# Kernel tuning notes

Measured on AMD Instinct MI355X. Metric: run time of the kernel, lower is better.

Reference implementation:

```python
import jax, jax.numpy as jnp
import numpy as np

N = 100000
E = 3200000
H = 128
C = 40


def setup_inputs() -> dict:
    key = jax.random.key(0)
    ks = jax.random.split(key, 7)
    x = jax.random.normal(ks[0], (N, H), dtype=jnp.float32)
    edge_src = jax.random.randint(ks[1], (E,), 0, N, dtype=jnp.int32)
    edge_dst = jnp.sort(jax.random.randint(ks[2], (E,), 0, N, dtype=jnp.int32))
    edge_w = jax.random.uniform(ks[3], (E,), dtype=jnp.float32)
    s = 1.0 / np.sqrt(H)
    W0 = jax.random.normal(ks[4], (H, H), dtype=jnp.float32) * s
    W1 = jax.random.normal(ks[5], (H, H), dtype=jnp.float32) * s
    W2 = jax.random.normal(ks[6], (H, C), dtype=jnp.float32) * s
    return {"x": x, "edge_src": edge_src, "edge_dst": edge_dst,
            "edge_w": edge_w, "W0": W0, "W1": W1, "W2": W2}


def _spmm(h, edge_src, edge_dst, edge_w):
    # out[i] = sum_{e: dst_e == i} w_e * h[src_e]   (sparse adj @ h)
    msgs = h[edge_src] * edge_w[:, None]          # [E, d]
    return jax.ops.segment_sum(msgs, edge_dst, num_segments=N)


def reference(x, edge_src, edge_dst, edge_w, W0, W1, W2):
    # layer 1: tanh(Linear(spmm(adj, x)))  (dropout is identity in eval mode)
    h = jnp.tanh(_spmm(x, edge_src, edge_dst, edge_w) @ W0)
    # layer 2
    h = jnp.tanh(_spmm(h, edge_src, edge_dst, edge_w) @ W1)
    # output layer (GraphConvSparse default activation is tanh here too)
    out = jnp.tanh(_spmm(h, edge_src, edge_dst, edge_w) @ W2)
    return out
```

## Files before the change

### kernel.cpp

```cpp
#include <hip/hip_runtime.h>
#include <hip/hip_fp16.h>

#define NN 100000
#define NPAD 100096
#define EE 3200000
#define HH 128
#define CC 40
#define NT 16

typedef _Float16 f16x8 __attribute__((ext_vector_type(8)));
typedef float f32x4 __attribute__((ext_vector_type(4)));

#define EDEC_W(v) ((float)((v) >> 17) * (1.f / 32767.f))
#define EDEC_S(v) ((v) & 131071u)

__device__ __forceinline__ float fast_tanh(float x) {
    float t = __expf(2.f * fminf(x, 15.f));
    return (t - 1.f) * __builtin_amdgcn_rcpf(t + 1.f);
}

__global__ void build_rp(const int* __restrict__ dst, int* __restrict__ rp) {
    int i = blockIdx.x * blockDim.x + threadIdx.x;
    if (i > NN) return;
    int lo = 0, hi = EE;
    while (lo < hi) {
        int mid = (lo + hi) >> 1;
        if (dst[mid] < i) lo = mid + 1; else hi = mid;
    }
    rp[i] = lo;
}

__global__ __launch_bounds__(256) void prep_all(const float* __restrict__ x,
                                                const int* __restrict__ src,
                                                const float* __restrict__ w,
                                                const float* __restrict__ W0,
                                                const float* __restrict__ W1,
                                                const float* __restrict__ W2,
                                                __half* __restrict__ xh,
                                                unsigned* __restrict__ ewp,
                                                __half* __restrict__ W0t,
                                                __half* __restrict__ W1t,
                                                __half* __restrict__ W2t) {
    int b = blockIdx.x, tid = threadIdx.x;
    if (b < 6250) {
        int base = (b * 256 + tid) * 8;
        float4 a = *(const float4*)(x + base);
        float4 c = *(const float4*)(x + base + 4);
        __half2 h[4];
        h[0] = __floats2half2_rn(a.x, a.y);
        h[1] = __floats2half2_rn(a.z, a.w);
        h[2] = __floats2half2_rn(c.x, c.y);
        h[3] = __floats2half2_rn(c.z, c.w);
        *(float4*)(xh + base) = *(float4*)h;
    } else if (b < 9375) {
        int i = (b - 6250) * 256 + tid;
        int4 s = ((const int4*)src)[i];
        float4 f = ((const float4*)w)[i];
        uint4 p;
        p.x = (unsigned)s.x | ((unsigned)(f.x * 32767.f + 0.5f) << 17);
        p.y = (unsigned)s.y | ((unsigned)(f.y * 32767.f + 0.5f) << 17);
        p.z = (unsigned)s.z | ((unsigned)(f.z * 32767.f + 0.5f) << 17);
        p.w = (unsigned)s.w | ((unsigned)(f.w * 32767.f + 0.5f) << 17);
        ((uint4*)ewp)[i] = p;
    } else {
        int i = (b - 9375) * 256 + tid;
        if (i < HH * HH) {
            int c = i >> 7, k = i & 127;
            W0t[i] = __float2half_rn(W0[k * HH + c]);
            W1t[i] = __float2half_rn(W1[k * HH + c]);
        }
        if (i < 64 * HH) {
            int c = i >> 7, k = i & 127;
            W2t[i] = __float2half_rn(c < CC ? W2[k * CC + c] : 0.f);
        }
    }
}

__global__ __launch_bounds__(256) void sort_edges(const unsigned* __restrict__ in,
                                                  const int* __restrict__ rp,
                                                  unsigned* __restrict__ outp) {
    int node = blockIdx.x * 4 + (threadIdx.x >> 6);
    int l = threadIdx.x & 63;
    if (node >= NN) return;
    int e0 = __builtin_amdgcn_readfirstlane(rp[node]);
    int e1 = __builtin_amdgcn_readfirstlane(rp[node + 1]);
    int count[NT];
#pragma unroll
    for (int t = 0; t < NT; ++t) count[t] = 0;
    for (int e = e0; e < e1; e += 64) {
        int idx = e + l;
        bool val = idx < e1;
        unsigned v = val ? in[idx] : 0u;
        int t = val ? (int)(EDEC_S(v) >> 13) : -1;
#pragma unroll
        for (int tt = 0; tt < NT; ++tt)
            count[tt] += __popcll(__ballot(t == tt));
    }
    int base[NT];
    int run = e0;
#pragma unroll
    for (int tt = 0; tt < NT; ++tt) { base[tt] = run; run += count[tt]; }
    unsigned long long lmask = (1ull << l) - 1ull;
    for (int e = e0; e < e1; e += 64) {
        int idx = e + l;
        bool val = idx < e1;
        unsigned v = val ? in[idx] : 0u;
        int t = val ? (int)(EDEC_S(v) >> 13) : -1;
#pragma unroll
        for (int tt = 0; tt < NT; ++tt) {
            unsigned long long b = __ballot(t == tt);
            if (t == tt) outp[base[tt] + __popcll(b & lmask)] = v;
            base[tt] += __popcll(b);
        }
    }
}

__global__ __launch_bounds__(256) void spmm_h16(const __half* __restrict__ h,
                                                const unsigned* __restrict__ ewp,
                                                const int* __restrict__ rp,
                                                __half* __restrict__ out) {
    int node = blockIdx.x * 4 + (threadIdx.x >> 6);
    int l = threadIdx.x & 63;
    if (node >= NN) return;
    int e0 = __builtin_amdgcn_readfirstlane(rp[node]);
    int e1 = __builtin_amdgcn_readfirstlane(rp[node + 1]);
    int g = l >> 4, r = l & 15;
    const f16x8* __restrict__ hrow = (const f16x8*)h;
    float acc[8] = {};
    int e = e0;
    while ((e & 3) && e < e1) {
        unsigned v = ewp[e];
        float wk = (g == 0) ? EDEC_W(v) : 0.f;
        f16x8 vv = hrow[(size_t)EDEC_S(v) * 16 + r];
#pragma unroll
        for (int j = 0; j < 8; ++j) acc[j] = fmaf(wk, (float)vv[j], acc[j]);
        ++e;
    }
    int e16 = e + ((e1 - e) & ~15);
    for (; e < e16; e += 16) {
        uint4 p = *(const uint4*)(ewp + e + 4 * g);
        f16x8 v0 = hrow[(size_t)EDEC_S(p.x) * 16 + r];
        f16x8 v1 = hrow[(size_t)EDEC_S(p.y) * 16 + r];
        f16x8 v2 = hrow[(size_t)EDEC_S(p.z) * 16 + r];
        f16x8 v3 = hrow[(size_t)EDEC_S(p.w) * 16 + r];
        float w0 = EDEC_W(p.x), w1 = EDEC_W(p.y), w2 = EDEC_W(p.z), w3 = EDEC_W(p.w);
#pragma unroll
        for (int j = 0; j < 8; ++j) acc[j] = fmaf(w0, (float)v0[j], acc[j]);
#pragma unroll
        for (int j = 0; j < 8; ++j) acc[j] = fmaf(w1, (float)v1[j], acc[j]);
#pragma unroll
        for (int j = 0; j < 8; ++j) acc[j] = fmaf(w2, (float)v2[j], acc[j]);
#pragma unroll
        for (int j = 0; j < 8; ++j) acc[j] = fmaf(w3, (float)v3[j], acc[j]);
    }
    if (e < e1) {
#pragma unroll
        for (int k = 0; k < 4; ++k) {
            int idx = e + 4 * g + k;
            bool val = idx < e1;
            unsigned v = ewp[val ? idx : e0];
            float wk = val ? EDEC_W(v) : 0.f;
            f16x8 vv = hrow[(size_t)EDEC_S(v) * 16 + r];
#pragma unroll
            for (int j = 0; j < 8; ++j) acc[j] = fmaf(wk, (float)vv[j], acc[j]);
        }
    }
#pragma unroll
    for (int j = 0; j < 8; ++j) {
        acc[j] += __shfl_xor(acc[j], 16);
        acc[j] += __shfl_xor(acc[j], 32);
    }
    if (l < 16) {
        __half2 hv[4];
#pragma unroll
        for (int j = 0; j < 4; ++j) hv[j] = __floats2half2_rn(acc[2 * j], acc[2 * j + 1]);
        *(float4*)(out + (size_t)node * HH + r * 8) = *(float4*)hv;
    }
}

__global__ __launch_bounds__(256) void spmm40_tanh(const __half* __restrict__ gpad,
                                                   const unsigned* __restrict__ ewp,
                                                   const int* __restrict__ rp,
                                                   float* __restrict__ out) {
    int node = blockIdx.x * 4 + (threadIdx.x >> 6);
    int l = threadIdx.x & 63;
    if (node >= NN) return;
    int e0 = __builtin_amdgcn_readfirstlane(rp[node]);
    int e1 = __builtin_amdgcn_readfirstlane(rp[node + 1]);
    int g = l >> 3, r = l & 7;
    const f16x8* __restrict__ grw = (const f16x8*)gpad;
    float acc[8] = {};
    int e = e0;
    while ((e & 1) && e < e1) {
        unsigned v = ewp[e];
        float wk = (g == 0) ? EDEC_W(v) : 0.f;
        f16x8 vv = grw[(size_t)EDEC_S(v) * 8 + r];
#pragma unroll
        for (int j = 0; j < 8; ++j) acc[j] = fmaf(wk, (float)vv[j], acc[j]);
        ++e;
    }
    int e16 = e + ((e1 - e) & ~15);
    for (; e < e16; e += 16) {
        uint2 pa = *(const uint2*)(ewp + e + 2 * g);
        f16x8 v0 = grw[(size_t)EDEC_S(pa.x) * 8 + r];
        f16x8 v1 = grw[(size_t)EDEC_S(pa.y) * 8 + r];
        float w0 = EDEC_W(pa.x), w1 = EDEC_W(pa.y);
#pragma unroll
        for (int j = 0; j < 8; ++j) acc[j] = fmaf(w0, (float)v0[j], acc[j]);
#pragma unroll
        for (int j = 0; j < 8; ++j) acc[j] = fmaf(w1, (float)v1[j], acc[j]);
    }
    if (e < e1) {
#pragma unroll
        for (int k = 0; k < 2; ++k) {
            int idx = e + 2 * g + k;
            bool val = idx < e1;
            unsigned v = ewp[val ? idx : e0];
            float wk = val ? EDEC_W(v) : 0.f;
            f16x8 vv = grw[(size_t)EDEC_S(v) * 8 + r];
#pragma unroll
            for (int j = 0; j < 8; ++j) acc[j] = fmaf(wk, (float)vv[j], acc[j]);
        }
    }
#pragma unroll
    for (int j = 0; j < 8; ++j) {
        acc[j] += __shfl_xor(acc[j], 8);
        acc[j] += __shfl_xor(acc[j], 16);
        acc[j] += __shfl_xor(acc[j], 32);
    }
    if (l < 5) {
        float o[8];
#pragma unroll
        for (int j = 0; j < 8; ++j) o[j] = fast_tanh(acc[j]);
        *(float4*)(out + (size_t)node * CC + r * 8) = *(float4*)&o[0];
        *(float4*)(out + (size_t)node * CC + r * 8 + 4) = *(float4*)&o[4];
    }
}

__global__ __launch_bounds__(256) void gemm_tanh_mfma(const __half* __restrict__ A,
                                                      const __half* __restrict__ Wt,
                                                      __half* __restrict__ out) {
    __shared__ _Float16 st[4][16][136];
    int wave = threadIdx.x >> 6, l = threadIdx.x & 63;
    int r0 = blockIdx.x * 64 + wave * 16;
    int lr = l & 15, lg = l >> 4;
    const _Float16* Af = (const _Float16*)A;
    const _Float16* Wf = (const _Float16*)Wt;
    f16x8 a[4];
#pragma unroll
    for (int kb = 0; kb < 4; ++kb)
        a[kb] = *(const f16x8*)(Af + (size_t)(r0 + lr) * HH + kb * 32 + lg * 8);
#pragma unroll
    for (int ct = 0; ct < 8; ++ct) {
        f32x4 acc = {0.f, 0.f, 0.f, 0.f};
#pragma unroll
        for (int kb = 0; kb < 4; ++kb) {
            f16x8 b = *(const f16x8*)(Wf + (size_t)(ct * 16 + lr) * HH + kb * 32 + lg * 8);
            acc = __builtin_amdgcn_mfma_f32_16x16x32_f16(a[kb], b, acc, 0, 0, 0);
        }
#pragma unroll
        for (int r = 0; r < 4; ++r)
            st[wave][lg * 4 + r][ct * 16 + lr] = (_Float16)fast_tanh(acc[r]);
    }
#pragma unroll
    for (int i = 0; i < 4; ++i) {
        int row = lg + 4 * i;
        int grow = r0 + row;
        f16x8 v = *(const f16x8*)&st[wave][row][lr * 8];
        if (grow < NN)
            *(f16x8*)((_Float16*)out + (size_t)grow * HH + lr * 8) = v;
    }
}

__global__ __launch_bounds__(256) void gemm2_fused(const __half* __restrict__ A,
                                                   const __half* __restrict__ W1t,
                                                   const __half* __restrict__ W2t,
                                                   __half* __restrict__ gout) {
    __shared__ _Float16 st[4][16][136];
    int wave = threadIdx.x >> 6, l = threadIdx.x & 63;
    int r0 = blockIdx.x * 64 + wave * 16;
    int lr = l & 15, lg = l >> 4;
    const _Float16* Af = (const _Float16*)A;
    const _Float16* W1f = (const _Float16*)W1t;
    const _Float16* W2f = (const _Float16*)W2t;
    f16x8 a[4];
#pragma unroll
    for (int kb = 0; kb < 4; ++kb)
        a[kb] = *(const f16x8*)(Af + (size_t)(r0 + lr) * HH + kb * 32 + lg * 8);
#pragma unroll
    for (int ct = 0; ct < 8; ++ct) {
        f32x4 acc = {0.f, 0.f, 0.f, 0.f};
#pragma unroll
        for (int kb = 0; kb < 4; ++kb) {
            f16x8 b = *(const f16x8*)(W1f + (size_t)(ct * 16 + lr) * HH + kb * 32 + lg * 8);
            acc = __builtin_amdgcn_mfma_f32_16x16x32_f16(a[kb], b, acc, 0, 0, 0);
        }
#pragma unroll
        for (int r = 0; r < 4; ++r)
            st[wave][lg * 4 + r][ct * 16 + lr] = (_Float16)fast_tanh(acc[r]);
    }
    f16x8 a2[4];
#pragma unroll
    for (int kb = 0; kb < 4; ++kb)
        a2[kb] = *(const f16x8*)&st[wave][lr][kb * 32 + lg * 8];
#pragma unroll
    for (int ct = 0; ct < 4; ++ct) {
        f32x4 acc = {0.f, 0.f, 0.f, 0.f};
#pragma unroll
        for (int kb = 0; kb < 4; ++kb) {
            f16x8 b = *(const f16x8*)(W2f + (size_t)(ct * 16 + lr) * HH + kb * 32 + lg * 8);
            acc = __builtin_amdgcn_mfma_f32_16x16x32_f16(a2[kb], b, acc, 0, 0, 0);
        }
#pragma unroll
        for (int r = 0; r < 4; ++r)
            st[wave][lg * 4 + r][ct * 16 + lr] = (_Float16)acc[r];
    }
#pragma unroll
    for (int i = 0; i < 2; ++i) {
        int row = (l >> 3) + 8 * i;
        int grow = r0 + row;
        f16x8 v = *(const f16x8*)&st[wave][row][(l & 7) * 8];
        if (grow < NN)
            *(f16x8*)((_Float16*)gout + (size_t)grow * 64 + (l & 7) * 8) = v;
    }
}

extern "C" void kernel_launch(void* const* d_in, const int* in_sizes, int n_in,
                              void* d_out, int out_size, void* d_ws, size_t ws_size,
                              hipStream_t stream) {
    const float* x    = (const float*)d_in[0];
    const int*   esrc = (const int*)d_in[1];
    const int*   edst = (const int*)d_in[2];
    const float* ew_f = (const float*)d_in[3];
    const float* W0   = (const float*)d_in[4];
    const float* W1   = (const float*)d_in[5];
    const float* W2   = (const float*)d_in[6];
    float* out = (float*)d_out;

    char* ws = (char*)d_ws;
    size_t off = 0;
    int* rp = (int*)(ws + off);            off += (((size_t)(NN + 1) * 4) + 511) & ~(size_t)511;
    __half* buf0 = (__half*)(ws + off);    off += (size_t)NPAD * HH * sizeof(__half);
    __half* sA = (__half*)(ws + off);      off += (size_t)NPAD * HH * sizeof(__half);
    __half* hb = (__half*)(ws + off);      off += (size_t)NPAD * HH * sizeof(__half);
    unsigned* ewp = (unsigned*)(ws + off); off += (size_t)EE * sizeof(unsigned);
    unsigned* ews = (unsigned*)(ws + off); off += (size_t)EE * sizeof(unsigned);
    __half* W0t = (__half*)(ws + off);     off += (size_t)HH * HH * sizeof(__half);
    __half* W1t = (__half*)(ws + off);     off += (size_t)HH * HH * sizeof(__half);
    __half* W2t = (__half*)(ws + off);     off += (size_t)64 * HH * sizeof(__half);
    __half* xh = buf0;
    __half* gb = buf0;

    build_rp<<<(NN + 256) / 256, 256, 0, stream>>>(edst, rp);
    prep_all<<<9440, 256, 0, stream>>>(x, esrc, ew_f, W0, W1, W2,
                                       xh, ewp, W0t, W1t, W2t);
    sort_edges<<<NN / 4, 256, 0, stream>>>(ewp, rp, ews);

    int gemm_grid = NPAD / 64;
    spmm_h16<<<NN / 4, 256, 0, stream>>>(xh, ews, rp, sA);
    gemm_tanh_mfma<<<gemm_grid, 256, 0, stream>>>(sA, W0t, hb);
    spmm_h16<<<NN / 4, 256, 0, stream>>>(hb, ews, rp, sA);
    gemm2_fused<<<gemm_grid, 256, 0, stream>>>(sA, W1t, W2t, gb);
    spmm40_tanh<<<NN / 4, 256, 0, stream>>>(gb, ews, rp, out);
}
```

Before: 504.7 us.

## Fuse SpMM with dense GEMM per layer and drop the edge-sorting pass

Each of the first two layers now runs as one kernel: each 512-thread block aggregates 16 node rows into LDS, then applies the MFMA GEMM and tanh directly from LDS. This removes the intermediate sA buffer round-trips through global memory and two kernel launches. The row-pointer binary search moves into the prep kernel, and the per-node sort of edges by source tile is removed, which saves a full pass over the edge list. The cost is that gathers now follow the original edge order, so cache locality on the source-row reads may be worse.

```diff
diff --git a/kernel.cpp b/kernel.cpp
--- a/kernel.cpp
+++ b/kernel.cpp
@@ -2,13 +2,12 @@
 #include <hip/hip_fp16.h>
 
 #define NN 100000
-#define NPAD 100096
 #define EE 3200000
 #define HH 128
 #define CC 40
-#define NT 16
 
 typedef _Float16 f16x8 __attribute__((ext_vector_type(8)));
+typedef _Float16 f16x4 __attribute__((ext_vector_type(4)));
 typedef float f32x4 __attribute__((ext_vector_type(4)));
 
 #define EDEC_W(v) ((float)((v) >> 17) * (1.f / 32767.f))
@@ -19,19 +18,9 @@
     return (t - 1.f) * __builtin_amdgcn_rcpf(t + 1.f);
 }
 
-__global__ void build_rp(const int* __restrict__ dst, int* __restrict__ rp) {
-    int i = blockIdx.x * blockDim.x + threadIdx.x;
-    if (i > NN) return;
-    int lo = 0, hi = EE;
-    while (lo < hi) {
-        int mid = (lo + hi) >> 1;
-        if (dst[mid] < i) lo = mid + 1; else hi = mid;
-    }
-    rp[i] = lo;
-}
-
 __global__ __launch_bounds__(256) void prep_all(const float* __restrict__ x,
                                                 const int* __restrict__ src,
+                                                const int* __restrict__ dst,
                                                 const float* __restrict__ w,
                                                 const float* __restrict__ W0,
                                                 const float* __restrict__ W1,
@@ -40,7 +29,8 @@
                                                 unsigned* __restrict__ ewp,
                                                 __half* __restrict__ W0t,
                                                 __half* __restrict__ W1t,
-                                                __half* __restrict__ W2t) {
+                                                __half* __restrict__ W2t,
+                                                int* __restrict__ rp) {
     int b = blockIdx.x, tid = threadIdx.x;
     if (b < 6250) {
         int base = (b * 256 + tid) * 8;
@@ -62,7 +52,7 @@
         p.z = (unsigned)s.z | ((unsigned)(f.z * 32767.f + 0.5f) << 17);
         p.w = (unsigned)s.w | ((unsigned)(f.w * 32767.f + 0.5f) << 17);
         ((uint4*)ewp)[i] = p;
-    } else {
+    } else if (b < 9440) {
         int i = (b - 9375) * 256 + tid;
         if (i < HH * HH) {
             int c = i >> 7, k = i & 127;
@@ -73,108 +63,170 @@
             int c = i >> 7, k = i & 127;
             W2t[i] = __float2half_rn(c < CC ? W2[k * CC + c] : 0.f);
         }
-    }
-}
-
-__global__ __launch_bounds__(256) void sort_edges(const unsigned* __restrict__ in,
-                                                  const int* __restrict__ rp,
-                                                  unsigned* __restrict__ outp) {
-    int node = blockIdx.x * 4 + (threadIdx.x >> 6);
-    int l = threadIdx.x & 63;
-    if (node >= NN) return;
-    int e0 = __builtin_amdgcn_readfirstlane(rp[node]);
-    int e1 = __builtin_amdgcn_readfirstlane(rp[node + 1]);
-    int count[NT];
-#pragma unroll
-    for (int t = 0; t < NT; ++t) count[t] = 0;
-    for (int e = e0; e < e1; e += 64) {
-        int idx = e + l;
-        bool val = idx < e1;
-        unsigned v = val ? in[idx] : 0u;
-        int t = val ? (int)(EDEC_S(v) >> 13) : -1;
-#pragma unroll
-        for (int tt = 0; tt < NT; ++tt)
-            count[tt] += __popcll(__ballot(t == tt));
-    }
-    int base[NT];
-    int run = e0;
-#pragma unroll
-    for (int tt = 0; tt < NT; ++tt) { base[tt] = run; run += count[tt]; }
-    unsigned long long lmask = (1ull << l) - 1ull;
-    for (int e = e0; e < e1; e += 64) {
-        int idx = e + l;
-        bool val = idx < e1;
-        unsigned v = val ? in[idx] : 0u;
-        int t = val ? (int)(EDEC_S(v) >> 13) : -1;
-#pragma unroll
-        for (int tt = 0; tt < NT; ++tt) {
-            unsigned long long b = __ballot(t == tt);
-            if (t == tt) outp[base[tt] + __popcll(b & lmask)] = v;
-            base[tt] += __popcll(b);
-        }
-    }
-}
-
-__global__ __launch_bounds__(256) void spmm_h16(const __half* __restrict__ h,
-                                                const unsigned* __restrict__ ewp,
-                                                const int* __restrict__ rp,
-                                                __half* __restrict__ out) {
-    int node = blockIdx.x * 4 + (threadIdx.x >> 6);
-    int l = threadIdx.x & 63;
-    if (node >= NN) return;
-    int e0 = __builtin_amdgcn_readfirstlane(rp[node]);
-    int e1 = __builtin_amdgcn_readfirstlane(rp[node + 1]);
+    } else {
+        int i = (b - 9440) * 256 + tid;
+        if (i > NN) return;
+        int lo = 0, hi = EE;
+        while (lo < hi) {
+            int mid = (lo + hi) >> 1;
+            if (dst[mid] < i) lo = mid + 1; else hi = mid;
+        }
+        rp[i] = lo;
+    }
+}
+
+__device__ __forceinline__ void spmm_2nodes(const f16x8* __restrict__ hrow,
+                                            const unsigned* __restrict__ ewp,
+                                            const int* __restrict__ rp,
+                                            int n0, int wave, int l,
+                                            _Float16 (* __restrict__ As)[136]) {
     int g = l >> 4, r = l & 15;
-    const f16x8* __restrict__ hrow = (const f16x8*)h;
-    float acc[8] = {};
-    int e = e0;
-    while ((e & 3) && e < e1) {
-        unsigned v = ewp[e];
-        float wk = (g == 0) ? EDEC_W(v) : 0.f;
-        f16x8 vv = hrow[(size_t)EDEC_S(v) * 16 + r];
-#pragma unroll
-        for (int j = 0; j < 8; ++j) acc[j] = fmaf(wk, (float)vv[j], acc[j]);
-        ++e;
-    }
-    int e16 = e + ((e1 - e) & ~15);
-    for (; e < e16; e += 16) {
-        uint4 p = *(const uint4*)(ewp + e + 4 * g);
-        f16x8 v0 = hrow[(size_t)EDEC_S(p.x) * 16 + r];
-        f16x8 v1 = hrow[(size_t)EDEC_S(p.y) * 16 + r];
-        f16x8 v2 = hrow[(size_t)EDEC_S(p.z) * 16 + r];
-        f16x8 v3 = hrow[(size_t)EDEC_S(p.w) * 16 + r];
-        float w0 = EDEC_W(p.x), w1 = EDEC_W(p.y), w2 = EDEC_W(p.z), w3 = EDEC_W(p.w);
-#pragma unroll
-        for (int j = 0; j < 8; ++j) acc[j] = fmaf(w0, (float)v0[j], acc[j]);
-#pragma unroll
-        for (int j = 0; j < 8; ++j) acc[j] = fmaf(w1, (float)v1[j], acc[j]);
-#pragma unroll
-        for (int j = 0; j < 8; ++j) acc[j] = fmaf(w2, (float)v2[j], acc[j]);
-#pragma unroll
-        for (int j = 0; j < 8; ++j) acc[j] = fmaf(w3, (float)v3[j], acc[j]);
-    }
-    if (e < e1) {
-#pragma unroll
-        for (int k = 0; k < 4; ++k) {
-            int idx = e + 4 * g + k;
-            bool val = idx < e1;
-            unsigned v = ewp[val ? idx : e0];
-            float wk = val ? EDEC_W(v) : 0.f;
+#pragma unroll 1
+    for (int p = 0; p < 2; ++p) {
+        int node = n0 + wave * 2 + p;
+        int e0 = __builtin_amdgcn_readfirstlane(rp[node]);
+        int e1 = __builtin_amdgcn_readfirstlane(rp[node + 1]);
+        float acc[8] = {};
+        int e = e0;
+        while ((e & 3) && e < e1) {
+            unsigned v = ewp[e];
+            float wk = (g == 0) ? EDEC_W(v) : 0.f;
             f16x8 vv = hrow[(size_t)EDEC_S(v) * 16 + r];
 #pragma unroll
             for (int j = 0; j < 8; ++j) acc[j] = fmaf(wk, (float)vv[j], acc[j]);
-        }
-    }
-#pragma unroll
-    for (int j = 0; j < 8; ++j) {
-        acc[j] += __shfl_xor(acc[j], 16);
-        acc[j] += __shfl_xor(acc[j], 32);
-    }
-    if (l < 16) {
-        __half2 hv[4];
-#pragma unroll
-        for (int j = 0; j < 4; ++j) hv[j] = __floats2half2_rn(acc[2 * j], acc[2 * j + 1]);
-        *(float4*)(out + (size_t)node * HH + r * 8) = *(float4*)hv;
+            ++e;
+        }
+        int e16 = e + ((e1 - e) & ~15);
+#pragma unroll 1
+        for (; e < e16; e += 16) {
+            uint4 pk = *(const uint4*)(ewp + e + 4 * g);
+            f16x8 v0 = hrow[(size_t)EDEC_S(pk.x) * 16 + r];
+            f16x8 v1 = hrow[(size_t)EDEC_S(pk.y) * 16 + r];
+            f16x8 v2 = hrow[(size_t)EDEC_S(pk.z) * 16 + r];
+            f16x8 v3 = hrow[(size_t)EDEC_S(pk.w) * 16 + r];
+            float w0 = EDEC_W(pk.x), w1 = EDEC_W(pk.y);
+            float w2 = EDEC_W(pk.z), w3 = EDEC_W(pk.w);
+#pragma unroll
+            for (int j = 0; j < 8; ++j) acc[j] = fmaf(w0, (float)v0[j], acc[j]);
+#pragma unroll
+            for (int j = 0; j < 8; ++j) acc[j] = fmaf(w1, (float)v1[j], acc[j]);
+#pragma unroll
+            for (int j = 0; j < 8; ++j) acc[j] = fmaf(w2, (float)v2[j], acc[j]);
+#pragma unroll
+            for (int j = 0; j < 8; ++j) acc[j] = fmaf(w3, (float)v3[j], acc[j]);
+        }
+        if (e < e1) {
+#pragma unroll
+            for (int k = 0; k < 4; ++k) {
+                int idx = e + 4 * g + k;
+                bool val = idx < e1;
+                unsigned v = ewp[val ? idx : e0];
+                float wk = val ? EDEC_W(v) : 0.f;
+                f16x8 vv = hrow[(size_t)EDEC_S(v) * 16 + r];
+#pragma unroll
+                for (int j = 0; j < 8; ++j) acc[j] = fmaf(wk, (float)vv[j], acc[j]);
+            }
+        }
+#pragma unroll
+        for (int j = 0; j < 8; ++j) {
+            acc[j] += __shfl_xor(acc[j], 16);
+            acc[j] += __shfl_xor(acc[j], 32);
+        }
+        if (l < 16) {
+            f16x8 vv;
+#pragma unroll
+            for (int j = 0; j < 8; ++j) vv[j] = (_Float16)acc[j];
+            *(f16x8*)&As[wave * 2 + p][r * 8] = vv;
+        }
+    }
+}
+
+__global__ __launch_bounds__(512, 6) void fused_l1(const __half* __restrict__ h,
+                                                   const unsigned* __restrict__ ewp,
+                                                   const int* __restrict__ rp,
+                                                   const __half* __restrict__ Wt,
+                                                   __half* __restrict__ out) {
+    __shared__ _Float16 As[16][136];
+    __shared__ _Float16 As2[16][136];
+    int tid = threadIdx.x, wave = tid >> 6, l = tid & 63;
+    int n0 = blockIdx.x * 16;
+    spmm_2nodes((const f16x8*)h, ewp, rp, n0, wave, l, As);
+    __syncthreads();
+    int lr = l & 15, lg = l >> 4;
+    const _Float16* Wf = (const _Float16*)Wt;
+    {
+        f16x8 a[4];
+#pragma unroll
+        for (int kb = 0; kb < 4; ++kb)
+            a[kb] = *(const f16x8*)&As[lr][kb * 32 + lg * 8];
+        f32x4 acc = {0.f, 0.f, 0.f, 0.f};
+#pragma unroll
+        for (int kb = 0; kb < 4; ++kb) {
+            f16x8 b = *(const f16x8*)(Wf + (size_t)(wave * 16 + lr) * HH + kb * 32 + lg * 8);
+            acc = __builtin_amdgcn_mfma_f32_16x16x32_f16(a[kb], b, acc, 0, 0, 0);
+        }
+#pragma unroll
+        for (int rr = 0; rr < 4; ++rr)
+            As2[lg * 4 + rr][wave * 16 + lr] = (_Float16)fast_tanh(acc[rr]);
+    }
+    __syncthreads();
+    int row = wave * 2 + (l >> 5), c = (l & 31) * 4;
+    f16x4 v = *(const f16x4*)&As2[row][c];
+    *(f16x4*)((_Float16*)out + (size_t)(n0 + row) * HH + c) = v;
+}
+
+__global__ __launch_bounds__(512, 6) void fused_l2(const __half* __restrict__ h,
+                                                   const unsigned* __restrict__ ewp,
+                                                   const int* __restrict__ rp,
+                                                   const __half* __restrict__ W1t,
+                                                   const __half* __restrict__ W2t,
+                                                   __half* __restrict__ gout) {
+    __shared__ _Float16 As[16][136];
+    __shared__ _Float16 As2[16][136];
+    int tid = threadIdx.x, wave = tid >> 6, l = tid & 63;
+    int n0 = blockIdx.x * 16;
+    spmm_2nodes((const f16x8*)h, ewp, rp, n0, wave, l, As);
+    __syncthreads();
+    int lr = l & 15, lg = l >> 4;
+    const _Float16* W1f = (const _Float16*)W1t;
+    const _Float16* W2f = (const _Float16*)W2t;
+    {
+        f16x8 a[4];
+#pragma unroll
+        for (int kb = 0; kb < 4; ++kb)
+            a[kb] = *(const f16x8*)&As[lr][kb * 32 + lg * 8];
+        f32x4 acc = {0.f, 0.f, 0.f, 0.f};
+#pragma unroll
+        for (int kb = 0; kb < 4; ++kb) {
+            f16x8 b = *(const f16x8*)(W1f + (size_t)(wave * 16 + lr) * HH + kb * 32 + lg * 8);
+            acc = __builtin_amdgcn_mfma_f32_16x16x32_f16(a[kb], b, acc, 0, 0, 0);
+        }
+#pragma unroll
+        for (int rr = 0; rr < 4; ++rr)
+            As2[lg * 4 + rr][wave * 16 + lr] = (_Float16)fast_tanh(acc[rr]);
+    }
+    __syncthreads();
+    if (wave < 4) {
+        f16x8 a[4];
+#pragma unroll
+        for (int kb = 0; kb < 4; ++kb)
+            a[kb] = *(const f16x8*)&As2[lr][kb * 32 + lg * 8];
+        f32x4 acc = {0.f, 0.f, 0.f, 0.f};
+#pragma unroll
+        for (int kb = 0; kb < 4; ++kb) {
+            f16x8 b = *(const f16x8*)(W2f + (size_t)(wave * 16 + lr) * HH + kb * 32 + lg * 8);
+            acc = __builtin_amdgcn_mfma_f32_16x16x32_f16(a[kb], b, acc, 0, 0, 0);
+        }
+#pragma unroll
+        for (int rr = 0; rr < 4; ++rr)
+            As[lg * 4 + rr][wave * 16 + lr] = (_Float16)acc[rr];
+    }
+    __syncthreads();
+    if (wave < 4) {
+        int row = wave * 4 + (l >> 4);
+        int c = (l & 15) * 4;
+        f16x4 v = *(const f16x4*)&As[row][c];
+        *(f16x4*)((_Float16*)gout + (size_t)(n0 + row) * 64 + c) = v;
     }
 }
 
@@ -237,94 +289,6 @@
     }
 }
 
-__global__ __launch_bounds__(256) void gemm_tanh_mfma(const __half* __restrict__ A,
-                                                      const __half* __restrict__ Wt,
-                                                      __half* __restrict__ out) {
-    __shared__ _Float16 st[4][16][136];
-    int wave = threadIdx.x >> 6, l = threadIdx.x & 63;
-    int r0 = blockIdx.x * 64 + wave * 16;
-    int lr = l & 15, lg = l >> 4;
-    const _Float16* Af = (const _Float16*)A;
-    const _Float16* Wf = (const _Float16*)Wt;
-    f16x8 a[4];
-#pragma unroll
-    for (int kb = 0; kb < 4; ++kb)
-        a[kb] = *(const f16x8*)(Af + (size_t)(r0 + lr) * HH + kb * 32 + lg * 8);
-#pragma unroll
-    for (int ct = 0; ct < 8; ++ct) {
-        f32x4 acc = {0.f, 0.f, 0.f, 0.f};
-#pragma unroll
-        for (int kb = 0; kb < 4; ++kb) {
-            f16x8 b = *(const f16x8*)(Wf + (size_t)(ct * 16 + lr) * HH + kb * 32 + lg * 8);
-            acc = __builtin_amdgcn_mfma_f32_16x16x32_f16(a[kb], b, acc, 0, 0, 0);
-        }
-#pragma unroll
-        for (int r = 0; r < 4; ++r)
-            st[wave][lg * 4 + r][ct * 16 + lr] = (_Float16)fast_tanh(acc[r]);
-    }
-#pragma unroll
-    for (int i = 0; i < 4; ++i) {
-        int row = lg + 4 * i;
-        int grow = r0 + row;
-        f16x8 v = *(const f16x8*)&st[wave][row][lr * 8];
-        if (grow < NN)
-            *(f16x8*)((_Float16*)out + (size_t)grow * HH + lr * 8) = v;
-    }
-}
-
-__global__ __launch_bounds__(256) void gemm2_fused(const __half* __restrict__ A,
-                                                   const __half* __restrict__ W1t,
-                                                   const __half* __restrict__ W2t,
-                                                   __half* __restrict__ gout) {
-    __shared__ _Float16 st[4][16][136];
-    int wave = threadIdx.x >> 6, l = threadIdx.x & 63;
-    int r0 = blockIdx.x * 64 + wave * 16;
-    int lr = l & 15, lg = l >> 4;
-    const _Float16* Af = (const _Float16*)A;
-    const _Float16* W1f = (const _Float16*)W1t;
-    const _Float16* W2f = (const _Float16*)W2t;
-    f16x8 a[4];
-#pragma unroll
-    for (int kb = 0; kb < 4; ++kb)
-        a[kb] = *(const f16x8*)(Af + (size_t)(r0 + lr) * HH + kb * 32 + lg * 8);
-#pragma unroll
-    for (int ct = 0; ct < 8; ++ct) {
-        f32x4 acc = {0.f, 0.f, 0.f, 0.f};
-#pragma unroll
-        for (int kb = 0; kb < 4; ++kb) {
-            f16x8 b = *(const f16x8*)(W1f + (size_t)(ct * 16 + lr) * HH + kb * 32 + lg * 8);
-            acc = __builtin_amdgcn_mfma_f32_16x16x32_f16(a[kb], b, acc, 0, 0, 0);
-        }
-#pragma unroll
-        for (int r = 0; r < 4; ++r)
-            st[wave][lg * 4 + r][ct * 16 + lr] = (_Float16)fast_tanh(acc[r]);
-    }
-    f16x8 a2[4];
-#pragma unroll
-    for (int kb = 0; kb < 4; ++kb)
-        a2[kb] = *(const f16x8*)&st[wave][lr][kb * 32 + lg * 8];
-#pragma unroll
-    for (int ct = 0; ct < 4; ++ct) {
-        f32x4 acc = {0.f, 0.f, 0.f, 0.f};
-#pragma unroll
-        for (int kb = 0; kb < 4; ++kb) {
-            f16x8 b = *(const f16x8*)(W2f + (size_t)(ct * 16 + lr) * HH + kb * 32 + lg * 8);
-            acc = __builtin_amdgcn_mfma_f32_16x16x32_f16(a2[kb], b, acc, 0, 0, 0);
-        }
-#pragma unroll
-        for (int r = 0; r < 4; ++r)
-            st[wave][lg * 4 + r][ct * 16 + lr] = (_Float16)acc[r];
-    }
-#pragma unroll
-    for (int i = 0; i < 2; ++i) {
-        int row = (l >> 3) + 8 * i;
-        int grow = r0 + row;
-        f16x8 v = *(const f16x8*)&st[wave][row][(l & 7) * 8];
-        if (grow < NN)
-            *(f16x8*)((_Float16*)gout + (size_t)grow * 64 + (l & 7) * 8) = v;
-    }
-}
-
 extern "C" void kernel_launch(void* const* d_in, const int* in_sizes, int n_in,
                               void* d_out, int out_size, void* d_ws, size_t ws_size,
                               hipStream_t stream) {
@@ -340,26 +304,19 @@
     char* ws = (char*)d_ws;
     size_t off = 0;
     int* rp = (int*)(ws + off);            off += (((size_t)(NN + 1) * 4) + 511) & ~(size_t)511;
-    __half* buf0 = (__half*)(ws + off);    off += (size_t)NPAD * HH * sizeof(__half);
-    __half* sA = (__half*)(ws + off);      off += (size_t)NPAD * HH * sizeof(__half);
-    __half* hb = (__half*)(ws + off);      off += (size_t)NPAD * HH * sizeof(__half);
+    __half* buf0 = (__half*)(ws + off);    off += (size_t)NN * HH * sizeof(__half);
+    __half* hb = (__half*)(ws + off);      off += (size_t)NN * HH * sizeof(__half);
     unsigned* ewp = (unsigned*)(ws + off); off += (size_t)EE * sizeof(unsigned);
-    unsigned* ews = (unsigned*)(ws + off); off += (size_t)EE * sizeof(unsigned);
     __half* W0t = (__half*)(ws + off);     off += (size_t)HH * HH * sizeof(__half);
     __half* W1t = (__half*)(ws + off);     off += (size_t)HH * HH * sizeof(__half);
     __half* W2t = (__half*)(ws + off);     off += (size_t)64 * HH * sizeof(__half);
     __half* xh = buf0;
     __half* gb = buf0;
 
-    build_rp<<<(NN + 256) / 256, 256, 0, stream>>>(edst, rp);
-    prep_all<<<9440, 256, 0, stream>>>(x, esrc, ew_f, W0, W1, W2,
-                                       xh, ewp, W0t, W1t, W2t);
-    sort_edges<<<NN / 4, 256, 0, stream>>>(ewp, rp, ews);
-
-    int gemm_grid = NPAD / 64;
-    spmm_h16<<<NN / 4, 256, 0, stream>>>(xh, ews, rp, sA);
-    gemm_tanh_mfma<<<gemm_grid, 256, 0, stream>>>(sA, W0t, hb);
-    spmm_h16<<<NN / 4, 256, 0, stream>>>(hb, ews, rp, sA);
-    gemm2_fused<<<gemm_grid, 256, 0, stream>>>(sA, W1t, W2t, gb);
-    spmm40_tanh<<<NN / 4, 256, 0, stream>>>(gb, ews, rp, out);
-}
+    prep_all<<<9832, 256, 0, stream>>>(x, esrc, edst, ew_f, W0, W1, W2,
+                                       xh, ewp, W0t, W1t, W2t, rp);
+
+    fused_l1<<<NN / 16, 512, 0, stream>>>(xh, ewp, rp, W0t, hb);
+    fused_l2<<<NN / 16, 512, 0, stream>>>(hb, ewp, rp, W1t, W2t, gb);
+    spmm40_tanh<<<NN / 4, 256, 0, stream>>>(gb, ewp, rp, out);
+}
```

Result: faster. 435.7 us (-13.7%).
